# Performance work log

Measured on AMD Instinct MI355X. Metric: run time of the kernel, lower is better.

Reference implementation:

```python
import jax, jax.numpy as jnp
import numpy as np


def setup_inputs() -> dict:
    key = jax.random.key(0)
    kb, kc = jax.random.split(key)
    B, P, N, D = 64, 8192, 128, 2
    batch = jax.random.uniform(kb, (B, P, D), dtype=jnp.float32)
    not_dummy = jnp.ones((B, P), dtype=jnp.float32)  # all points valid
    centers = jax.random.uniform(kc, (N, D), dtype=jnp.float32)
    sharpness = jnp.ones((N, D), dtype=jnp.float32) * 3.0  # default init: ones * 3
    return {"batch": batch, "not_dummy": not_dummy, "centers": centers, "sharpness": sharpness}


def reference(batch, not_dummy, centers, sharpness):
    # batch: [B, P, d]; not_dummy: [B, P]; centers/sharpness: [N, d]
    # RBF kernel per (batch, element, point): exp(-sum_d sharpness*(center-point)^2)
    diff = centers[None, :, None, :] - batch[:, None, :, :]          # [B, N, P, d]
    dist = jnp.sum(diff * diff * sharpness[None, :, None, :], axis=-1)  # [B, N, P]
    x = jnp.exp(-dist) * not_dummy[:, None, :]                        # mask dummy points
    out = jnp.sum(x, axis=-1)                                         # [B, N]
    return jnp.squeeze(out)
```

## Files before the change

### kernel.cpp

```cpp
#include <hip/hip_runtime.h>

#define THREADS 512
#define NTILE 8

#define S_CONST    12102203.161561485f
#define BIAS_CONST 1064872549.0f

static __device__ __forceinline__ float uni(float x) {
    return __int_as_float(__builtin_amdgcn_readfirstlane(__float_as_int(x)));
}

static __device__ __forceinline__ void body_iso(
    float x0, float x1, float mk,
    const float* cA, const float* cB, const float* cC, const float* cD,
    float* acc)
{
    const float r2 = __builtin_fmaf(x1, x1, x0 * x0);
#pragma unroll
    for (int i = 0; i < NTILE; ++i) {
        float t = __builtin_fmaf(cD[i], r2, cA[i]);
        t = __builtin_fmaf(cB[i], x0, t);
        t = __builtin_fmaf(cC[i], x1, t);
        acc[i] = __builtin_fmaf(__int_as_float((int)t), mk, acc[i]);
    }
}

static __device__ __forceinline__ void body_gen(
    float x0, float x1, float mk,
    const float* cA, const float* cB, const float* cC, const float* cD,
    const float* cE, float* acc)
{
    const float sq0 = x0 * x0, sq1 = x1 * x1;
#pragma unroll
    for (int i = 0; i < NTILE; ++i) {
        float t = __builtin_fmaf(cB[i], x0, cA[i]);
        t = __builtin_fmaf(cC[i], x1, t);
        t = __builtin_fmaf(cD[i], sq0, t);
        t = __builtin_fmaf(cE[i], sq1, t);
        acc[i] = __builtin_fmaf(__int_as_float((int)t), mk, acc[i]);
    }
}

template <bool ISO>
static __device__ __forceinline__ void main_loop(
    const float4* B4, const float4* M4, int quads, int tid,
    const float* cA, const float* cB, const float* cC, const float* cD,
    const float* cE, float* acc)
{
    int q = tid;
    if (q >= quads) return;
    float4 pa = B4[2 * q], pb = B4[2 * q + 1], pm = M4[q];
    while (true) {
        const int qn = q + THREADS;
        const bool vn = qn < quads;
        const int qc = vn ? qn : q;
        float4 na = B4[2 * qc], nb = B4[2 * qc + 1], nm = M4[qc];

        if (ISO) {
            body_iso(pa.x, pa.y, pm.x, cA, cB, cC, cD, acc);
            body_iso(pa.z, pa.w, pm.y, cA, cB, cC, cD, acc);
            body_iso(pb.x, pb.y, pm.z, cA, cB, cC, cD, acc);
            body_iso(pb.z, pb.w, pm.w, cA, cB, cC, cD, acc);
        } else {
            body_gen(pa.x, pa.y, pm.x, cA, cB, cC, cD, cE, acc);
            body_gen(pa.z, pa.w, pm.y, cA, cB, cC, cD, cE, acc);
            body_gen(pb.x, pb.y, pm.z, cA, cB, cC, cD, cE, acc);
            body_gen(pb.z, pb.w, pm.w, cA, cB, cC, cD, cE, acc);
        }

        if (!vn) break;
        q = qn; pa = na; pb = nb; pm = nm;
    }
}

__global__ __launch_bounds__(THREADS, 8) void slayer_exp_kernel(
    const float* __restrict__ batch,
    const float* __restrict__ not_dummy,
    const float* __restrict__ centers,
    const float* __restrict__ sharpness,
    float* __restrict__ out,
    int B, int P, int N, int T)
{
    const int id = blockIdx.x;
    int b, j;
    if ((B & 7) == 0) {
        const int r = id >> 3;
        j = r % T;
        b = (r / T) * 8 + (id & 7);
    } else {
        b = id / T;
        j = id % T;
    }
    const int n0  = j * NTILE;
    const int tid = threadIdx.x;

    float cA[NTILE], cB[NTILE], cC[NTILE], cD[NTILE], cE[NTILE];
    bool iso = true;
#pragma unroll
    for (int i = 0; i < NTILE; ++i) {
        int n = n0 + i; if (n >= N) n = N - 1;
        const float c0 = centers[2 * n], c1 = centers[2 * n + 1];
        const float s0 = sharpness[2 * n], s1 = sharpness[2 * n + 1];
        cA[i] = BIAS_CONST - S_CONST * (s0 * c0 * c0 + s1 * c1 * c1);
        cB[i] = uni(S_CONST * 2.0f * s0 * c0);
        cC[i] = uni(S_CONST * 2.0f * s1 * c1);
        cD[i] = uni(-S_CONST * s0);
        cE[i] = uni(-S_CONST * s1);
        iso = iso && (s0 == s1);
    }

    float acc[NTILE];
#pragma unroll
    for (int i = 0; i < NTILE; ++i) acc[i] = 0.0f;

    const float4* B4 = (const float4*)(batch + (size_t)b * P * 2);
    const float4* M4 = (const float4*)(not_dummy + (size_t)b * P);
    const int quads = P >> 2;

    if (iso) main_loop<true>(B4, M4, quads, tid, cA, cB, cC, cD, cE, acc);
    else     main_loop<false>(B4, M4, quads, tid, cA, cB, cC, cD, cE, acc);

    if ((P & 3) && tid == 0) {
        const float* bb = batch + (size_t)b * P * 2;
        const float* mm = not_dummy + (size_t)b * P;
        for (int p = (quads << 2); p < P; ++p)
            body_gen(bb[2 * p], bb[2 * p + 1], mm[p], cA, cB, cC, cD, cE, acc);
    }

#pragma unroll
    for (int i = 0; i < NTILE; ++i) {
        float v = acc[i];
#pragma unroll
        for (int off = 32; off >= 1; off >>= 1)
            v += __shfl_xor(v, off, 64);
        acc[i] = v;
    }

    __shared__ float red[THREADS / 64][NTILE];
    const int wave = tid >> 6;
    const int lane = tid & 63;
    if (lane == 0) {
#pragma unroll
        for (int i = 0; i < NTILE; ++i) red[wave][i] = acc[i];
    }
    __syncthreads();

    if (tid < NTILE && (n0 + tid) < N) {
        float v = 0.0f;
#pragma unroll
        for (int w = 0; w < THREADS / 64; ++w) v += red[w][tid];
        out[(size_t)b * N + n0 + tid] = v;
    }
}

extern "C" void kernel_launch(void* const* d_in, const int* in_sizes, int n_in,
                              void* d_out, int out_size, void* d_ws, size_t ws_size,
                              hipStream_t stream) {
    const float* batch     = (const float*)d_in[0];
    const float* not_dummy = (const float*)d_in[1];
    const float* centers   = (const float*)d_in[2];
    const float* sharp     = (const float*)d_in[3];
    float* out = (float*)d_out;

    const int N  = in_sizes[2] / 2;
    const int BP = in_sizes[1];
    const int B  = out_size / N;
    const int P  = BP / B;
    const int T  = (N + NTILE - 1) / NTILE;

    dim3 grid(T * B);
    slayer_exp_kernel<<<grid, THREADS, 0, stream>>>(batch, not_dummy, centers, sharp,
                                                    out, B, P, N, T);
}
```

Before: 17.88 us.

## Split point range across two blocks per tile with atomic accumulation

Each (batch, center-tile) pair is now handled by two 256-thread blocks, each covering half of the points, instead of one 512-thread block. The partial sums are combined with atomicAdd into an output that is zeroed by a hipMemsetAsync before launch. The aim is more, smaller blocks for better load balance and scheduling across CUs. The cost is an extra memset and atomic traffic, and the float summation order is no longer deterministic.

New measurement: 22.86 us. 27.8% more time.

```diff
diff --git a/kernel.cpp b/kernel.cpp
--- a/kernel.cpp
+++ b/kernel.cpp
@@ -1,6 +1,6 @@
 #include <hip/hip_runtime.h>
 
-#define THREADS 512
+#define THREADS 256
 #define NTILE 8
 
 #define S_CONST    12102203.161561485f
@@ -43,16 +43,16 @@
 
 template <bool ISO>
 static __device__ __forceinline__ void main_loop(
-    const float4* B4, const float4* M4, int quads, int tid,
+    const float4* B4, const float4* M4, int qlo, int qhi, int tid,
     const float* cA, const float* cB, const float* cC, const float* cD,
     const float* cE, float* acc)
 {
-    int q = tid;
-    if (q >= quads) return;
+    int q = qlo + tid;
+    if (q >= qhi) return;
     float4 pa = B4[2 * q], pb = B4[2 * q + 1], pm = M4[q];
     while (true) {
         const int qn = q + THREADS;
-        const bool vn = qn < quads;
+        const bool vn = qn < qhi;
         const int qc = vn ? qn : q;
         float4 na = B4[2 * qc], nb = B4[2 * qc + 1], nm = M4[qc];
 
@@ -82,14 +82,18 @@
     int B, int P, int N, int T)
 {
     const int id = blockIdx.x;
-    int b, j;
+    int b, j, half;
     if ((B & 7) == 0) {
+        const int xcd = id & 7;
         const int r = id >> 3;
         j = r % T;
-        b = (r / T) * 8 + (id & 7);
+        half = (r / T) & 1;
+        b = (r / (2 * T)) * 8 + xcd;
     } else {
-        b = id / T;
-        j = id % T;
+        b = id / (2 * T);
+        const int rem = id % (2 * T);
+        half = rem / T;
+        j = rem % T;
     }
     const int n0  = j * NTILE;
     const int tid = threadIdx.x;
@@ -115,15 +119,18 @@
 
     const float4* B4 = (const float4*)(batch + (size_t)b * P * 2);
     const float4* M4 = (const float4*)(not_dummy + (size_t)b * P);
-    const int quads = P >> 2;
+    const int quadsT = P >> 2;
+    const int qmid   = quadsT >> 1;
+    const int qlo    = half ? qmid : 0;
+    const int qhi    = half ? quadsT : qmid;
 
-    if (iso) main_loop<true>(B4, M4, quads, tid, cA, cB, cC, cD, cE, acc);
-    else     main_loop<false>(B4, M4, quads, tid, cA, cB, cC, cD, cE, acc);
+    if (iso) main_loop<true>(B4, M4, qlo, qhi, tid, cA, cB, cC, cD, cE, acc);
+    else     main_loop<false>(B4, M4, qlo, qhi, tid, cA, cB, cC, cD, cE, acc);
 
-    if ((P & 3) && tid == 0) {
+    if ((P & 3) && half == 1 && tid == 0) {
         const float* bb = batch + (size_t)b * P * 2;
         const float* mm = not_dummy + (size_t)b * P;
-        for (int p = (quads << 2); p < P; ++p)
+        for (int p = (quadsT << 2); p < P; ++p)
             body_gen(bb[2 * p], bb[2 * p + 1], mm[p], cA, cB, cC, cD, cE, acc);
     }
 
@@ -149,7 +156,7 @@
         float v = 0.0f;
 #pragma unroll
         for (int w = 0; w < THREADS / 64; ++w) v += red[w][tid];
-        out[(size_t)b * N + n0 + tid] = v;
+        atomicAdd(&out[(size_t)b * N + n0 + tid], v);
     }
 }
 
@@ -168,7 +175,9 @@
     const int P  = BP / B;
     const int T  = (N + NTILE - 1) / NTILE;
 
-    dim3 grid(T * B);
+    hipMemsetAsync(out, 0, (size_t)out_size * sizeof(float), stream);
+
+    dim3 grid(T * B * 2);
     slayer_exp_kernel<<<grid, THREADS, 0, stream>>>(batch, not_dummy, centers, sharp,
                                                     out, B, P, N, T);
 }
```
